# Performance work log

Hardware: AMD Instinct MI355X
Metric: run time of the kernel (lower is better)

The kernel has to match this reference:

```python
import jax, jax.numpy as jnp
import numpy as np

N_NODES = 50000
N_EDGES = 1600000
IN_F = 256
OUT_F = 128
ALPHA = 0.2  # LeakyReLU negative slope
EPS = 1e-9


def setup_inputs() -> dict:
    key = jax.random.key(0)
    k1, k2, k3, k4 = jax.random.split(key, 4)
    x = jax.random.normal(k1, (N_NODES, IN_F), dtype=jnp.float32)
    edge_index = jax.random.randint(k2, (2, N_EDGES), 0, N_NODES, dtype=jnp.int64)
    # xavier_uniform-ish scale for params
    W = jax.random.normal(k3, (IN_F, OUT_F), dtype=jnp.float32) * (1.414 / np.sqrt(IN_F + OUT_F))
    a = jax.random.normal(k4, (1, 2 * OUT_F), dtype=jnp.float32) * (1.414 / np.sqrt(1 + 2 * OUT_F))
    return {"x": x, "edge_index": edge_index, "W": W, "a": a}


def reference(x, edge_index, W, a):
    N = x.shape[0]
    F = W.shape[1]
    h = x @ W                                  # [N, F]
    src = edge_index[0]                        # row indices (aggregation target)
    dst = edge_index[1]                        # col indices (neighbor source)
    a_src = a[0, :F]                           # split a.mm(cat(h_src, h_dst).T)
    a_dst = a[0, F:]
    score = h[src] @ a_src + h[dst] @ a_dst    # [E]
    e = jnp.exp(-jax.nn.leaky_relu(score, negative_slope=ALPHA))  # [E]
    # e_rowsum = A @ ones : sum of edge values per row
    rowsum = jax.ops.segment_sum(e, src, num_segments=N)          # [N]
    # h_prime = A @ h : weighted neighbor aggregation per row
    agg = jax.ops.segment_sum(e[:, None] * h[dst], src, num_segments=N)  # [N, F]
    h_prime = agg / (rowsum[:, None] + EPS)
    return jax.nn.elu(h_prime)  # concat=True -> elu
```

## Files before the change

kernel.cpp:

```cpp
#include <hip/hip_runtime.h>
#include <hip/hip_bf16.h>
#include <math.h>

#define N_NODES 50000
#define N_EDGES 1600000
#define IN_F 256
#define OUT_F 128
#define ALPHA 0.2f
#define EPS 1e-9f

#define NPB 32
#define BINS 1563
#define SUBCAP 1536
#define MAXDEG 128
#define PTILE 8192
#define PGRID ((N_EDGES + PTILE - 1) / PTILE)

#define GROWS 32
#define XPITCH 264

typedef __attribute__((ext_vector_type(8))) short short8v;
typedef __attribute__((ext_vector_type(4))) float f32x4;

__device__ __forceinline__ unsigned short bf16r(float f) {
  unsigned u = __float_as_uint(f);
  u = (u + 0x7FFFu + ((u >> 16) & 1u)) >> 16;
  return (unsigned short)u;
}

__device__ __forceinline__ unsigned pk2(float a, float b) {
  unsigned ua = (__float_as_uint(a) + 0x8000u) >> 16;
  unsigned ub = (__float_as_uint(b) + 0x8000u) & 0xFFFF0000u;
  return ua | ub;
}

__global__ __launch_bounds__(256) void wcvt_k(const float* __restrict__ W,
                                              unsigned short* __restrict__ Bf) {
  int fid = blockIdx.x * 256 + threadIdx.x;
  int lane = fid & 63;
  int ks = (fid >> 6) & 7;
  int cg = (fid >> 9) & 1;
  int wv = fid >> 10;
  int col = wv * 32 + cg * 16 + (lane & 15);
  int k0 = ks * 32 + (lane >> 4) * 8;
  unsigned short v[8];
#pragma unroll
  for (int j = 0; j < 8; ++j)
    v[j] = bf16r(W[(size_t)(k0 + j) * OUT_F + col]);
  *reinterpret_cast<short8v*>(&Bf[(size_t)fid * 8]) = *reinterpret_cast<short8v*>(v);
}

__global__ __launch_bounds__(256) void gemm_mfma(const float* __restrict__ x,
                                                 const unsigned short* __restrict__ Bf,
                                                 const float* __restrict__ a,
                                                 unsigned short* __restrict__ hbs,
                                                 float* __restrict__ s1,
                                                 float* __restrict__ s2) {
  __shared__ unsigned short xsb[GROWS][XPITCH];
  __shared__ float s1p[GROWS], s2p[GROWS];
  const int t = threadIdx.x;
  const int lane = t & 63;
  const int wv = t >> 6;
  const int row0 = blockIdx.x * GROWS;
  const int wcol0 = wv * 32;
  const int lrow = lane & 15;
  const int hi = lane >> 4;
  const int lk = hi * 8;

  if (t < GROWS) { s1p[t] = 0.f; s2p[t] = 0.f; }

#pragma unroll
  for (int it = 0; it < 8; ++it) {
    int f4 = it * 256 + t;
    int row = f4 >> 6;
    int c4 = (f4 & 63) * 4;
    int gr = row0 + row;
    if (gr >= N_NODES) gr = N_NODES - 1;
    float4 u = *reinterpret_cast<const float4*>(&x[(size_t)gr * IN_F + c4]);
    unsigned* p = reinterpret_cast<unsigned*>(&xsb[row][c4]);
    p[0] = pk2(u.x, u.y);
    p[1] = pk2(u.z, u.w);
  }

  short8v b[2][8];
#pragma unroll
  for (int cg = 0; cg < 2; ++cg)
#pragma unroll
    for (int ks = 0; ks < 8; ++ks)
      b[cg][ks] = *reinterpret_cast<const short8v*>(
          &Bf[(size_t)(((wv * 2 + cg) * 8 + ks) * 64 + lane) * 8]);

  float4 a1v = *reinterpret_cast<const float4*>(&a[wcol0 + 4 * hi]);
  float4 a1w = *reinterpret_cast<const float4*>(&a[wcol0 + 16 + 4 * hi]);
  float4 a2v = *reinterpret_cast<const float4*>(&a[128 + wcol0 + 4 * hi]);
  float4 a2w = *reinterpret_cast<const float4*>(&a[128 + wcol0 + 16 + 4 * hi]);
  __syncthreads();

#pragma unroll
  for (int rg = 0; rg < GROWS / 16; ++rg) {
    short8v av[8];
#pragma unroll
    for (int ks = 0; ks < 8; ++ks)
      av[ks] = *reinterpret_cast<const short8v*>(&xsb[rg * 16 + lrow][ks * 32 + lk]);
    f32x4 acc0 = {0.f, 0.f, 0.f, 0.f};
    f32x4 acc1 = {0.f, 0.f, 0.f, 0.f};
#pragma unroll
    for (int ks = 0; ks < 8; ++ks) {
      acc0 = __builtin_amdgcn_mfma_f32_16x16x32_bf16(b[0][ks], av[ks], acc0, 0, 0, 0);
      acc1 = __builtin_amdgcn_mfma_f32_16x16x32_bf16(b[1][ks], av[ks], acc1, 0, 0, 0);
    }
    int xrow = row0 + rg * 16 + lrow;
    if (xrow < N_NODES) {
      uint2 o0 = {pk2(acc0[0], acc0[1]), pk2(acc0[2], acc0[3])};
      uint2 o1 = {pk2(acc1[0], acc1[1]), pk2(acc1[2], acc1[3])};
      *reinterpret_cast<uint2*>(&hbs[(size_t)xrow * OUT_F + wcol0 + 4 * hi]) = o0;
      *reinterpret_cast<uint2*>(&hbs[(size_t)xrow * OUT_F + wcol0 + 16 + 4 * hi]) = o1;
    }
    float p1 = acc0[0] * a1v.x + acc0[1] * a1v.y + acc0[2] * a1v.z + acc0[3] * a1v.w
             + acc1[0] * a1w.x + acc1[1] * a1w.y + acc1[2] * a1w.z + acc1[3] * a1w.w;
    float p2 = acc0[0] * a2v.x + acc0[1] * a2v.y + acc0[2] * a2v.z + acc0[3] * a2v.w
             + acc1[0] * a2w.x + acc1[1] * a2w.y + acc1[2] * a2w.z + acc1[3] * a2w.w;
    p1 += __shfl_xor(p1, 16, 64);
    p2 += __shfl_xor(p2, 16, 64);
    p1 += __shfl_xor(p1, 32, 64);
    p2 += __shfl_xor(p2, 32, 64);
    if (hi == 0) {
      atomicAdd(&s1p[rg * 16 + lrow], p1);
      atomicAdd(&s2p[rg * 16 + lrow], p2);
    }
  }
  __syncthreads();
  if (t < GROWS) {
    int g = row0 + t;
    if (g < N_NODES) { s1[g] = s1p[t]; s2[g] = s2p[t]; }
  }
}

__device__ __forceinline__ int load_idx(const int* __restrict__ ei32, int isI64,
                                        long long pos) {
  if (isI64) return (int)(reinterpret_cast<const long long*>(ei32)[pos]);
  return ei32[pos];
}

__global__ __launch_bounds__(512) void part_k(const int* __restrict__ ei,
                                              unsigned* __restrict__ bins,
                                              int* __restrict__ bincur) {
  __shared__ int hist[BINS], cur[BINS], gbase[BINS];
  __shared__ int sf64;
  const int t = threadIdx.x;
  if (t < 64) {
    int nz = 0;
#pragma unroll
    for (int j = 0; j < 4; ++j) nz |= ei[2 * (t + j * 64) + 1];
    unsigned long long any = __ballot(nz != 0);
    if (t == 0) sf64 = (any == 0ull) ? 1 : 0;
  }
  for (int i = t; i < BINS; i += 512) hist[i] = 0;
  __syncthreads();
  const int f64 = sf64;
  const int base = blockIdx.x * PTILE;
  unsigned rec[16];
#pragma unroll
  for (int j = 0; j < 16; ++j) {
    int e = base + j * 512 + t;
    if (e < N_EDGES) {
      unsigned s = (unsigned)load_idx(ei, f64, e);
      unsigned d = (unsigned)load_idx(ei, f64, (long long)N_EDGES + e);
      rec[j] = (s << 16) | d;
      atomicAdd(&hist[s >> 5], 1);
    } else rec[j] = 0xFFFFFFFFu;
  }
  __syncthreads();
  for (int i = t; i < BINS; i += 512) {
    gbase[i] = hist[i] ? atomicAdd(&bincur[i], hist[i]) : 0;
    cur[i] = 0;
  }
  __syncthreads();
#pragma unroll
  for (int j = 0; j < 16; ++j) {
    if (rec[j] != 0xFFFFFFFFu) {
      int bb = rec[j] >> 21;
      int pos = atomicAdd(&cur[bb], 1);
      int o = gbase[bb] + pos;
      if (o < SUBCAP) bins[(size_t)bb * SUBCAP + o] = rec[j];
    }
  }
}

__global__ __launch_bounds__(512) void aggc_k(const unsigned* __restrict__ bins,
                                              const int* __restrict__ bincur,
                                              const float* __restrict__ s1,
                                              const float* __restrict__ s2,
                                              const unsigned* __restrict__ hb,
                                              float* __restrict__ out) {
  __shared__ unsigned short sorted[SUBCAP];
  __shared__ uint2 ebuf[8][MAXDEG];
  __shared__ int hist[NPB], cur[NPB], rowptr[NPB + 1];
  const int t = threadIdx.x;
  const int b = blockIdx.x;
  const int lo = b * NPB;
  const int n_b = min(bincur[b], SUBCAP);
  const unsigned* bp = bins + (size_t)b * SUBCAP;

  if (t < NPB) hist[t] = 0;
  __syncthreads();
  unsigned rec[3];
#pragma unroll
  for (int r = 0; r < 3; ++r) {
    int i = t + r * 512;
    rec[r] = 0xFFFFFFFFu;
    if (i < n_b) {
      rec[r] = bp[i];
      atomicAdd(&hist[(rec[r] >> 16) & (NPB - 1)], 1);
    }
  }
  __syncthreads();
  if (t < NPB) {
    int c = hist[t];
    int incl = c;
#pragma unroll
    for (int off = 1; off < NPB; off <<= 1) {
      int v = __shfl_up(incl, off, 64);
      if (t >= off) incl += v;
    }
    rowptr[t + 1] = incl;
    cur[t] = incl - c;
    if (t == 0) rowptr[0] = 0;
  }
  __syncthreads();
#pragma unroll
  for (int r = 0; r < 3; ++r) {
    if (rec[r] != 0xFFFFFFFFu) {
      int sl = (rec[r] >> 16) & (NPB - 1);
      int pos = atomicAdd(&cur[sl], 1);
      sorted[pos] = (unsigned short)(rec[r] & 0xFFFFu);
    }
  }
  __syncthreads();

  const int wv = t >> 6, lane = t & 63;
  for (int i = 0; i < 4; ++i) {
    int nl = wv * 4 + i;
    int g = lo + nl;
    if (g >= N_NODES) continue;
    int rp = rowptr[nl];
    int cn = min(rowptr[nl + 1] - rp, MAXDEG);
    float s1u = s1[g];
    float rsl = 0.f;
    for (int j = lane; j < cn; j += 64) {
      unsigned d = sorted[rp + j];
      float sc = s1u + s2[d];
      float w = __expf(-fmaxf(sc, ALPHA * sc));
      ebuf[wv][j] = make_uint2(d << 6, __float_as_uint(w));
      rsl += w;
    }
#pragma unroll
    for (int m = 32; m >= 1; m >>= 1) rsl += __shfl_xor(rsl, m, 64);
    float accx = 0.f, accy = 0.f;
    int j = 0;
    for (; j + 7 < cn; j += 8) {
      uint4 e0 = *reinterpret_cast<const uint4*>(&ebuf[wv][j]);
      uint4 e1 = *reinterpret_cast<const uint4*>(&ebuf[wv][j + 2]);
      uint4 e2 = *reinterpret_cast<const uint4*>(&ebuf[wv][j + 4]);
      uint4 e3 = *reinterpret_cast<const uint4*>(&ebuf[wv][j + 6]);
      unsigned v0 = hb[e0.x | lane];
      unsigned v1 = hb[e0.z | lane];
      unsigned v2 = hb[e1.x | lane];
      unsigned v3 = hb[e1.z | lane];
      unsigned v4 = hb[e2.x | lane];
      unsigned v5 = hb[e2.z | lane];
      unsigned v6 = hb[e3.x | lane];
      unsigned v7 = hb[e3.z | lane];
      float w0 = __uint_as_float(e0.y), w1 = __uint_as_float(e0.w);
      float w2 = __uint_as_float(e1.y), w3 = __uint_as_float(e1.w);
      float w4 = __uint_as_float(e2.y), w5 = __uint_as_float(e2.w);
      float w6 = __uint_as_float(e3.y), w7 = __uint_as_float(e3.w);
      accx = fmaf(w0, __uint_as_float(v0 << 16), accx);
      accy = fmaf(w0, __uint_as_float(v0 & 0xFFFF0000u), accy);
      accx = fmaf(w1, __uint_as_float(v1 << 16), accx);
      accy = fmaf(w1, __uint_as_float(v1 & 0xFFFF0000u), accy);
      accx = fmaf(w2, __uint_as_float(v2 << 16), accx);
      accy = fmaf(w2, __uint_as_float(v2 & 0xFFFF0000u), accy);
      accx = fmaf(w3, __uint_as_float(v3 << 16), accx);
      accy = fmaf(w3, __uint_as_float(v3 & 0xFFFF0000u), accy);
      accx = fmaf(w4, __uint_as_float(v4 << 16), accx);
      accy = fmaf(w4, __uint_as_float(v4 & 0xFFFF0000u), accy);
      accx = fmaf(w5, __uint_as_float(v5 << 16), accx);
      accy = fmaf(w5, __uint_as_float(v5 & 0xFFFF0000u), accy);
      accx = fmaf(w6, __uint_as_float(v6 << 16), accx);
      accy = fmaf(w6, __uint_as_float(v6 & 0xFFFF0000u), accy);
      accx = fmaf(w7, __uint_as_float(v7 << 16), accx);
      accy = fmaf(w7, __uint_as_float(v7 & 0xFFFF0000u), accy);
    }
    for (; j < cn; ++j) {
      uint2 e = ebuf[wv][j];
      unsigned v0 = hb[e.x | lane];
      float w0 = __uint_as_float(e.y);
      accx = fmaf(w0, __uint_as_float(v0 << 16), accx);
      accy = fmaf(w0, __uint_as_float(v0 & 0xFFFF0000u), accy);
    }
    float inv = 1.0f / (rsl + EPS);
    float px = accx * inv, py = accy * inv;
    px = px > 0.f ? px : expm1f(px);
    py = py > 0.f ? py : expm1f(py);
    float2 o = {px, py};
    *reinterpret_cast<float2*>(&out[(size_t)g * OUT_F + 2 * lane]) = o;
  }
}

extern "C" void kernel_launch(void* const* d_in, const int* in_sizes, int n_in,
                              void* d_out, int out_size, void* d_ws, size_t ws_size,
                              hipStream_t stream) {
  const float* x = (const float*)d_in[0];
  const int* ei = (const int*)d_in[1];
  const float* W = (const float*)d_in[2];
  const float* a = (const float*)d_in[3];
  float* out = (float*)d_out;

  unsigned* hb = (unsigned*)d_ws;
  float* s1 = (float*)(hb + (size_t)N_NODES * 64);
  float* s2 = s1 + N_NODES;
  int* bincur = (int*)(s2 + N_NODES);
  unsigned* bins = (unsigned*)(bincur + BINS);
  unsigned short* Bf = (unsigned short*)(bins + (size_t)BINS * SUBCAP);

  hipMemsetAsync(bincur, 0, (size_t)BINS * sizeof(int), stream);

  wcvt_k<<<16, 256, 0, stream>>>(W, Bf);
  gemm_mfma<<<(N_NODES + GROWS - 1) / GROWS, 256, 0, stream>>>(x, Bf, a, (unsigned short*)hb, s1, s2);
  part_k<<<PGRID, 512, 0, stream>>>(ei, bins, bincur);
  aggc_k<<<BINS, 512, 0, stream>>>(bins, bincur, s1, s2, hb, out);
}
```

Before: 106.1 us.

## Fuse edge partitioning and GEMM into one horizontally fused launch

Merges the edge-binning kernel and the MFMA GEMM kernel into a single launch, with the first block range doing partitioning and the rest doing GEMM rows. Shared memory is unioned between the two roles, and partition blocks now use 256 threads over tiles of 4096 edges. This removes one kernel launch and lets the memory-bound partition work overlap with GEMM blocks. In exchange, every block reserves the larger union LDS footprint, which may lower occupancy for the GEMM blocks.

```diff
diff --git a/kernel.cpp b/kernel.cpp
--- a/kernel.cpp
+++ b/kernel.cpp
@@ -13,10 +13,12 @@
 #define BINS 1563
 #define SUBCAP 1536
 #define MAXDEG 128
-#define PTILE 8192
-#define PGRID ((N_EDGES + PTILE - 1) / PTILE)
+
+#define PTILE2 4096
+#define PBLKS ((N_EDGES + PTILE2 - 1) / PTILE2)
 
 #define GROWS 32
+#define GBLKS ((N_NODES + GROWS - 1) / GROWS)
 #define XPITCH 264
 
 typedef __attribute__((ext_vector_type(8))) short short8v;
@@ -50,24 +52,86 @@
   *reinterpret_cast<short8v*>(&Bf[(size_t)fid * 8]) = *reinterpret_cast<short8v*>(v);
 }
 
-__global__ __launch_bounds__(256) void gemm_mfma(const float* __restrict__ x,
-                                                 const unsigned short* __restrict__ Bf,
-                                                 const float* __restrict__ a,
-                                                 unsigned short* __restrict__ hbs,
-                                                 float* __restrict__ s1,
-                                                 float* __restrict__ s2) {
-  __shared__ unsigned short xsb[GROWS][XPITCH];
-  __shared__ float s1p[GROWS], s2p[GROWS];
+__device__ __forceinline__ int load_idx(const int* __restrict__ ei32, int isI64,
+                                        long long pos) {
+  if (isI64) return (int)(reinterpret_cast<const long long*>(ei32)[pos]);
+  return ei32[pos];
+}
+
+union SMemU {
+  struct {
+    unsigned short xsb[GROWS][XPITCH];
+    float s1p[GROWS], s2p[GROWS];
+  } g;
+  struct {
+    int hist[BINS], cur[BINS], gbase[BINS];
+    int sf64;
+  } p;
+};
+
+__global__ __launch_bounds__(256) void fused_k(const float* __restrict__ x,
+                                               const unsigned short* __restrict__ Bf,
+                                               const float* __restrict__ a,
+                                               unsigned short* __restrict__ hbs,
+                                               float* __restrict__ s1,
+                                               float* __restrict__ s2,
+                                               const int* __restrict__ ei,
+                                               unsigned* __restrict__ bins,
+                                               int* __restrict__ bincur) {
+  __shared__ SMemU sm;
   const int t = threadIdx.x;
+
+  if (blockIdx.x < PBLKS) {
+    if (t < 64) {
+      int nz = 0;
+#pragma unroll
+      for (int j = 0; j < 4; ++j) nz |= ei[2 * (t + j * 64) + 1];
+      unsigned long long any = __ballot(nz != 0);
+      if (t == 0) sm.p.sf64 = (any == 0ull) ? 1 : 0;
+    }
+    for (int i = t; i < BINS; i += 256) sm.p.hist[i] = 0;
+    __syncthreads();
+    const int f64 = sm.p.sf64;
+    const int base = blockIdx.x * PTILE2;
+    unsigned rec[16];
+#pragma unroll
+    for (int j = 0; j < 16; ++j) {
+      int e = base + j * 256 + t;
+      if (e < N_EDGES) {
+        unsigned s = (unsigned)load_idx(ei, f64, e);
+        unsigned d = (unsigned)load_idx(ei, f64, (long long)N_EDGES + e);
+        rec[j] = (s << 16) | d;
+        atomicAdd(&sm.p.hist[s >> 5], 1);
+      } else rec[j] = 0xFFFFFFFFu;
+    }
+    __syncthreads();
+    for (int i = t; i < BINS; i += 256) {
+      sm.p.gbase[i] = sm.p.hist[i] ? atomicAdd(&bincur[i], sm.p.hist[i]) : 0;
+      sm.p.cur[i] = 0;
+    }
+    __syncthreads();
+#pragma unroll
+    for (int j = 0; j < 16; ++j) {
+      if (rec[j] != 0xFFFFFFFFu) {
+        int bb = rec[j] >> 21;
+        int pos = atomicAdd(&sm.p.cur[bb], 1);
+        int o = sm.p.gbase[bb] + pos;
+        if (o < SUBCAP) bins[(size_t)bb * SUBCAP + o] = rec[j];
+      }
+    }
+    return;
+  }
+
+  const int gbid = blockIdx.x - PBLKS;
   const int lane = t & 63;
   const int wv = t >> 6;
-  const int row0 = blockIdx.x * GROWS;
+  const int row0 = gbid * GROWS;
   const int wcol0 = wv * 32;
   const int lrow = lane & 15;
   const int hi = lane >> 4;
   const int lk = hi * 8;
 
-  if (t < GROWS) { s1p[t] = 0.f; s2p[t] = 0.f; }
+  if (t < GROWS) { sm.g.s1p[t] = 0.f; sm.g.s2p[t] = 0.f; }
 
 #pragma unroll
   for (int it = 0; it < 8; ++it) {
@@ -77,7 +141,7 @@
     int gr = row0 + row;
     if (gr >= N_NODES) gr = N_NODES - 1;
     float4 u = *reinterpret_cast<const float4*>(&x[(size_t)gr * IN_F + c4]);
-    unsigned* p = reinterpret_cast<unsigned*>(&xsb[row][c4]);
+    unsigned* p = reinterpret_cast<unsigned*>(&sm.g.xsb[row][c4]);
     p[0] = pk2(u.x, u.y);
     p[1] = pk2(u.z, u.w);
   }
@@ -101,7 +165,7 @@
     short8v av[8];
 #pragma unroll
     for (int ks = 0; ks < 8; ++ks)
-      av[ks] = *reinterpret_cast<const short8v*>(&xsb[rg * 16 + lrow][ks * 32 + lk]);
+      av[ks] = *reinterpret_cast<const short8v*>(&sm.g.xsb[rg * 16 + lrow][ks * 32 + lk]);
     f32x4 acc0 = {0.f, 0.f, 0.f, 0.f};
     f32x4 acc1 = {0.f, 0.f, 0.f, 0.f};
 #pragma unroll
@@ -125,65 +189,14 @@
     p1 += __shfl_xor(p1, 32, 64);
     p2 += __shfl_xor(p2, 32, 64);
     if (hi == 0) {
-      atomicAdd(&s1p[rg * 16 + lrow], p1);
-      atomicAdd(&s2p[rg * 16 + lrow], p2);
+      atomicAdd(&sm.g.s1p[rg * 16 + lrow], p1);
+      atomicAdd(&sm.g.s2p[rg * 16 + lrow], p2);
     }
   }
   __syncthreads();
   if (t < GROWS) {
     int g = row0 + t;
-    if (g < N_NODES) { s1[g] = s1p[t]; s2[g] = s2p[t]; }
-  }
-}
-
-__device__ __forceinline__ int load_idx(const int* __restrict__ ei32, int isI64,
-                                        long long pos) {
-  if (isI64) return (int)(reinterpret_cast<const long long*>(ei32)[pos]);
-  return ei32[pos];
-}
-
-__global__ __launch_bounds__(512) void part_k(const int* __restrict__ ei,
-                                              unsigned* __restrict__ bins,
-                                              int* __restrict__ bincur) {
-  __shared__ int hist[BINS], cur[BINS], gbase[BINS];
-  __shared__ int sf64;
-  const int t = threadIdx.x;
-  if (t < 64) {
-    int nz = 0;
-#pragma unroll
-    for (int j = 0; j < 4; ++j) nz |= ei[2 * (t + j * 64) + 1];
-    unsigned long long any = __ballot(nz != 0);
-    if (t == 0) sf64 = (any == 0ull) ? 1 : 0;
-  }
-  for (int i = t; i < BINS; i += 512) hist[i] = 0;
-  __syncthreads();
-  const int f64 = sf64;
-  const int base = blockIdx.x * PTILE;
-  unsigned rec[16];
-#pragma unroll
-  for (int j = 0; j < 16; ++j) {
-    int e = base + j * 512 + t;
-    if (e < N_EDGES) {
-      unsigned s = (unsigned)load_idx(ei, f64, e);
-      unsigned d = (unsigned)load_idx(ei, f64, (long long)N_EDGES + e);
-      rec[j] = (s << 16) | d;
-      atomicAdd(&hist[s >> 5], 1);
-    } else rec[j] = 0xFFFFFFFFu;
-  }
-  __syncthreads();
-  for (int i = t; i < BINS; i += 512) {
-    gbase[i] = hist[i] ? atomicAdd(&bincur[i], hist[i]) : 0;
-    cur[i] = 0;
-  }
-  __syncthreads();
-#pragma unroll
-  for (int j = 0; j < 16; ++j) {
-    if (rec[j] != 0xFFFFFFFFu) {
-      int bb = rec[j] >> 21;
-      int pos = atomicAdd(&cur[bb], 1);
-      int o = gbase[bb] + pos;
-      if (o < SUBCAP) bins[(size_t)bb * SUBCAP + o] = rec[j];
-    }
+    if (g < N_NODES) { s1[g] = sm.g.s1p[t]; s2[g] = sm.g.s2p[t]; }
   }
 }
 
@@ -327,7 +340,7 @@
   hipMemsetAsync(bincur, 0, (size_t)BINS * sizeof(int), stream);
 
   wcvt_k<<<16, 256, 0, stream>>>(W, Bf);
-  gemm_mfma<<<(N_NODES + GROWS - 1) / GROWS, 256, 0, stream>>>(x, Bf, a, (unsigned short*)hb, s1, s2);
-  part_k<<<PGRID, 512, 0, stream>>>(ei, bins, bincur);
+  fused_k<<<PBLKS + GBLKS, 256, 0, stream>>>(x, Bf, a, (unsigned short*)hb,
+                                             s1, s2, ei, bins, bincur);
   aggc_k<<<BINS, 512, 0, stream>>>(bins, bincur, s1, s2, hb, out);
 }
```

Result: faster. 104.0 us (-2.0%).
